# Optimization experiments

Measured on AMD Instinct MI355X. Metric: run time of the kernel, lower is better.

## Reference

```python
import jax, jax.numpy as jnp
import numpy as np

N = 500000      # total nodes
C = 256         # channels
R = 4           # reduction
B = 1024        # number of graphs (segments)


def setup_inputs() -> dict:
    key = jax.random.key(0)
    k1, k2, k3, k4 = jax.random.split(key, 4)
    x = jax.random.normal(k1, (N, C), dtype=jnp.float32)
    batch = jnp.sort(jax.random.randint(k2, (N,), 0, B, dtype=jnp.int64))
    # shared MLP weights (Linear without bias); stored as [in, out] for x @ W
    w1 = jax.random.normal(k3, (C, C // R), dtype=jnp.float32) * (1.0 / np.sqrt(C))
    w2 = jax.random.normal(k4, (C // R, C), dtype=jnp.float32) * (1.0 / np.sqrt(C // R))
    return {"x": x, "batch": batch, "w1": w1, "w2": w2}


def reference(x, batch, w1, w2):
    # scatter reductions over graph ids (dim_size = B)
    sum_res = jax.ops.segment_sum(x, batch, num_segments=B)          # [B, C]
    max_res = jax.ops.segment_max(x, batch, num_segments=B)          # [B, C]
    counts = jax.ops.segment_sum(jnp.ones((x.shape[0],), x.dtype), batch, num_segments=B)
    # torch_scatter fills empty segments with 0; segment_max gives -inf
    max_res = jnp.where(counts[:, None] > 0, max_res, jnp.zeros_like(max_res))

    def mlp(h):  # shared bottleneck MLP: Linear -> ReLU -> Linear (no bias)
        return jnp.maximum(h @ w1, 0) @ w2

    y = jax.nn.relu(mlp(max_res) + mlp(sum_res))                     # [B, C]
    return x * y[batch]                                              # gather + gate
```

## Files before the change

### kernel.cpp

```cpp
#include <hip/hip_runtime.h>
#include <math.h>

#define CCH   256
#define CCH4  64
#define BSEG  1024
#define HID   64

__global__ __launch_bounds__(256) void seg_reduce_kernel(
    const float* __restrict__ x, const int* __restrict__ batch, int N,
    float* __restrict__ sum_res, float* __restrict__ max_res) {
  int seg = blockIdx.x;
  __shared__ int s_bounds[2];
  if (threadIdx.x < 2) {
    int tgt = seg + (int)threadIdx.x;
    int lo = 0, hi = N;
    while (lo < hi) {
      int mid = (lo + hi) >> 1;
      if (batch[mid] < tgt) lo = mid + 1; else hi = mid;
    }
    s_bounds[threadIdx.x] = lo;
  }
  __syncthreads();
  int start = s_bounds[0], end = s_bounds[1];

  int wave = threadIdx.x >> 6;
  int lane = threadIdx.x & 63;
  const float4* x4 = (const float4*)x;

  float4 s = make_float4(0.f, 0.f, 0.f, 0.f);
  float4 m = make_float4(-INFINITY, -INFINITY, -INFINITY, -INFINITY);
  for (int r = start + wave; r < end; r += 4) {
    float4 v = x4[(size_t)r * CCH4 + lane];
    s.x += v.x; s.y += v.y; s.z += v.z; s.w += v.w;
    m.x = fmaxf(m.x, v.x); m.y = fmaxf(m.y, v.y);
    m.z = fmaxf(m.z, v.z); m.w = fmaxf(m.w, v.w);
  }

  __shared__ float4 sh_s[4][CCH4];
  __shared__ float4 sh_m[4][CCH4];
  sh_s[wave][lane] = s;
  sh_m[wave][lane] = m;
  __syncthreads();

  if (wave == 0) {
    float4 ts = sh_s[0][lane];
    float4 tm = sh_m[0][lane];
    for (int w = 1; w < 4; ++w) {
      float4 os = sh_s[w][lane];
      float4 om = sh_m[w][lane];
      ts.x += os.x; ts.y += os.y; ts.z += os.z; ts.w += os.w;
      tm.x = fmaxf(tm.x, om.x); tm.y = fmaxf(tm.y, om.y);
      tm.z = fmaxf(tm.z, om.z); tm.w = fmaxf(tm.w, om.w);
    }
    if (start == end) tm = make_float4(0.f, 0.f, 0.f, 0.f);
    ((float4*)sum_res)[(size_t)seg * CCH4 + lane] = ts;
    ((float4*)max_res)[(size_t)seg * CCH4 + lane] = tm;
  }
}

__global__ __launch_bounds__(256) void mlp_kernel(
    const float* __restrict__ sum_res, const float* __restrict__ max_res,
    const float* __restrict__ w1, const float* __restrict__ w2,
    float* __restrict__ y) {
  int seg = blockIdx.x;
  int t = threadIdx.x;
  __shared__ float srow[CCH];
  __shared__ float mrow[CCH];
  __shared__ float hsum[HID];
  __shared__ float hmax[HID];

  srow[t] = sum_res[(size_t)seg * CCH + t];
  mrow[t] = max_res[(size_t)seg * CCH + t];
  __syncthreads();

  if (t < HID) {
    float acc = 0.f;
    #pragma unroll 8
    for (int k = 0; k < CCH; ++k) acc = fmaf(srow[k], w1[k * HID + t], acc);
    hsum[t] = fmaxf(acc, 0.f);
  } else if (t < 2 * HID) {
    int j = t - HID;
    float acc = 0.f;
    #pragma unroll 8
    for (int k = 0; k < CCH; ++k) acc = fmaf(mrow[k], w1[k * HID + j], acc);
    hmax[j] = fmaxf(acc, 0.f);
  }
  __syncthreads();

  float acc = 0.f;
  #pragma unroll 8
  for (int j = 0; j < HID; ++j) acc = fmaf(hsum[j] + hmax[j], w2[j * CCH + t], acc);
  y[(size_t)seg * CCH + t] = fmaxf(acc, 0.f);
}

__global__ __launch_bounds__(256) void gate_kernel(
    const float* __restrict__ x, const int* __restrict__ batch,
    const float* __restrict__ y, float* __restrict__ out, int total4) {
  int idx = blockIdx.x * blockDim.x + threadIdx.x;
  if (idx >= total4) return;
  int n = idx >> 6;
  int q = idx & 63;
  int b = batch[n];
  const float4* x4 = (const float4*)x;
  const float4* y4 = (const float4*)y;
  float4 xv = x4[idx];
  float4 yv = y4[b * CCH4 + q];
  float4 o;
  o.x = xv.x * yv.x; o.y = xv.y * yv.y; o.z = xv.z * yv.z; o.w = xv.w * yv.w;
  ((float4*)out)[idx] = o;
}

extern "C" void kernel_launch(void* const* d_in, const int* in_sizes, int n_in,
                              void* d_out, int out_size, void* d_ws, size_t ws_size,
                              hipStream_t stream) {
  const float* x     = (const float*)d_in[0];
  const int*   batch = (const int*)d_in[1];
  const float* w1    = (const float*)d_in[2];
  const float* w2    = (const float*)d_in[3];
  float* out = (float*)d_out;

  int N = in_sizes[1];

  float* sum_res = (float*)d_ws;
  float* max_res = sum_res + (size_t)BSEG * CCH;
  float* y       = max_res + (size_t)BSEG * CCH;

  seg_reduce_kernel<<<BSEG, 256, 0, stream>>>(x, batch, N, sum_res, max_res);
  mlp_kernel<<<BSEG, 256, 0, stream>>>(sum_res, max_res, w1, w2, y);

  int total4 = N * CCH4;
  int blocks = (total4 + 255) / 256;
  gate_kernel<<<blocks, 256, 0, stream>>>(x, batch, y, out, total4);
}
```

Baseline: 932.9 us.

## Fuse segment reduction with MLP, unroll reduce loop, nontemporal gate I/O

Merges the segment sum/max reduction and the bottleneck MLP into one kernel, so per-segment results stay in shared memory and no longer round-trip through global workspace or need a separate launch. The reduction loop is unrolled by two to keep two row loads in flight per wave, and a launch-bounds occupancy hint is added. The gate kernel now uses nontemporal loads and stores for the streamed x and out arrays so they do not evict the reused y table from cache. The MLP work now runs serially after each block's reduction, which may lengthen the tail of the fused kernel.

```diff
diff --git a/kernel.cpp b/kernel.cpp
--- a/kernel.cpp
+++ b/kernel.cpp
@@ -6,9 +6,12 @@
 #define BSEG  1024
 #define HID   64
 
-__global__ __launch_bounds__(256) void seg_reduce_kernel(
+typedef float v4 __attribute__((ext_vector_type(4)));
+
+__global__ __launch_bounds__(256, 4) void seg_reduce_mlp_kernel(
     const float* __restrict__ x, const int* __restrict__ batch, int N,
-    float* __restrict__ sum_res, float* __restrict__ max_res) {
+    const float* __restrict__ w1, const float* __restrict__ w2,
+    float* __restrict__ y) {
   int seg = blockIdx.x;
   __shared__ int s_bounds[2];
   if (threadIdx.x < 2) {
@@ -29,7 +32,18 @@
 
   float4 s = make_float4(0.f, 0.f, 0.f, 0.f);
   float4 m = make_float4(-INFINITY, -INFINITY, -INFINITY, -INFINITY);
-  for (int r = start + wave; r < end; r += 4) {
+  int r = start + wave;
+  for (; r + 4 < end; r += 8) {
+    float4 v0 = x4[(size_t)r * CCH4 + lane];
+    float4 v1 = x4[(size_t)(r + 4) * CCH4 + lane];
+    s.x += v0.x; s.y += v0.y; s.z += v0.z; s.w += v0.w;
+    m.x = fmaxf(m.x, v0.x); m.y = fmaxf(m.y, v0.y);
+    m.z = fmaxf(m.z, v0.z); m.w = fmaxf(m.w, v0.w);
+    s.x += v1.x; s.y += v1.y; s.z += v1.z; s.w += v1.w;
+    m.x = fmaxf(m.x, v1.x); m.y = fmaxf(m.y, v1.y);
+    m.z = fmaxf(m.z, v1.z); m.w = fmaxf(m.w, v1.w);
+  }
+  if (r < end) {
     float4 v = x4[(size_t)r * CCH4 + lane];
     s.x += v.x; s.y += v.y; s.z += v.z; s.w += v.w;
     m.x = fmaxf(m.x, v.x); m.y = fmaxf(m.y, v.y);
@@ -38,6 +52,11 @@
 
   __shared__ float4 sh_s[4][CCH4];
   __shared__ float4 sh_m[4][CCH4];
+  __shared__ float srow[CCH];
+  __shared__ float mrow[CCH];
+  __shared__ float hsum[HID];
+  __shared__ float hmax[HID];
+
   sh_s[wave][lane] = s;
   sh_m[wave][lane] = m;
   __syncthreads();
@@ -53,26 +72,12 @@
       tm.z = fmaxf(tm.z, om.z); tm.w = fmaxf(tm.w, om.w);
     }
     if (start == end) tm = make_float4(0.f, 0.f, 0.f, 0.f);
-    ((float4*)sum_res)[(size_t)seg * CCH4 + lane] = ts;
-    ((float4*)max_res)[(size_t)seg * CCH4 + lane] = tm;
+    ((float4*)srow)[lane] = ts;
+    ((float4*)mrow)[lane] = tm;
   }
-}
-
-__global__ __launch_bounds__(256) void mlp_kernel(
-    const float* __restrict__ sum_res, const float* __restrict__ max_res,
-    const float* __restrict__ w1, const float* __restrict__ w2,
-    float* __restrict__ y) {
-  int seg = blockIdx.x;
-  int t = threadIdx.x;
-  __shared__ float srow[CCH];
-  __shared__ float mrow[CCH];
-  __shared__ float hsum[HID];
-  __shared__ float hmax[HID];
-
-  srow[t] = sum_res[(size_t)seg * CCH + t];
-  mrow[t] = max_res[(size_t)seg * CCH + t];
   __syncthreads();
 
+  int t = threadIdx.x;
   if (t < HID) {
     float acc = 0.f;
     #pragma unroll 8
@@ -101,13 +106,12 @@
   int n = idx >> 6;
   int q = idx & 63;
   int b = batch[n];
-  const float4* x4 = (const float4*)x;
-  const float4* y4 = (const float4*)y;
-  float4 xv = x4[idx];
-  float4 yv = y4[b * CCH4 + q];
-  float4 o;
-  o.x = xv.x * yv.x; o.y = xv.y * yv.y; o.z = xv.z * yv.z; o.w = xv.w * yv.w;
-  ((float4*)out)[idx] = o;
+  const v4* x4 = (const v4*)x;
+  const v4* y4 = (const v4*)y;
+  v4 xv = __builtin_nontemporal_load(&x4[idx]);
+  v4 yv = y4[(size_t)b * CCH4 + q];
+  v4 o = xv * yv;
+  __builtin_nontemporal_store(o, (v4*)out + idx);
 }
 
 extern "C" void kernel_launch(void* const* d_in, const int* in_sizes, int n_in,
@@ -121,12 +125,9 @@
 
   int N = in_sizes[1];
 
-  float* sum_res = (float*)d_ws;
-  float* max_res = sum_res + (size_t)BSEG * CCH;
-  float* y       = max_res + (size_t)BSEG * CCH;
+  float* y = (float*)d_ws;
 
-  seg_reduce_kernel<<<BSEG, 256, 0, stream>>>(x, batch, N, sum_res, max_res);
-  mlp_kernel<<<BSEG, 256, 0, stream>>>(sum_res, max_res, w1, w2, y);
+  seg_reduce_mlp_kernel<<<BSEG, 256, 0, stream>>>(x, batch, N, w1, w2, y);
 
   int total4 = N * CCH4;
   int blocks = (total4 + 255) / 256;
```

Result: faster. 895.7 us (-4.0%).
